# Kernel tuning notes

Measured on AMD Instinct MI355X. Metric: run time of the kernel, lower is better.

The kernel has to match this reference:

```python
import math
import jax, jax.numpy as jnp
import numpy as np

D_MODEL = 1024
D_K = 64
D_V = 64
N_HEADS = 16
D_HIDDEN = 4096
EPS = 1e-5


def setup_inputs() -> dict:
    key = jax.random.key(0)
    ks = jax.random.split(key, 10)
    s = 0.02
    x = jax.random.normal(ks[0], (2, 2048, D_MODEL), dtype=jnp.float32)
    wq = jax.random.normal(ks[1], (D_MODEL, D_K * N_HEADS), jnp.float32) * s
    bq = jnp.zeros((D_K * N_HEADS,), jnp.float32)
    wk = jax.random.normal(ks[2], (D_MODEL, D_K * N_HEADS), jnp.float32) * s
    bk = jnp.zeros((D_K * N_HEADS,), jnp.float32)
    wv = jax.random.normal(ks[3], (D_MODEL, D_V * N_HEADS), jnp.float32) * s
    bv = jnp.zeros((D_V * N_HEADS,), jnp.float32)
    wo = jax.random.normal(ks[4], (D_V * N_HEADS, D_MODEL), jnp.float32) * s
    ln1_g = jnp.ones((D_MODEL,), jnp.float32)
    ln1_b = jnp.zeros((D_MODEL,), jnp.float32)
    w1 = jax.random.normal(ks[5], (D_MODEL, D_HIDDEN), jnp.float32) * s
    b1 = jnp.zeros((D_HIDDEN,), jnp.float32)
    w2 = jax.random.normal(ks[6], (D_HIDDEN, D_MODEL), jnp.float32) * s
    ln2_g = jnp.ones((D_MODEL,), jnp.float32)
    ln2_b = jnp.zeros((D_MODEL,), jnp.float32)
    return dict(x=x, wq=wq, bq=bq, wk=wk, bk=bk, wv=wv, bv=bv, wo=wo,
                ln1_g=ln1_g, ln1_b=ln1_b, w1=w1, b1=b1, w2=w2,
                ln2_g=ln2_g, ln2_b=ln2_b)


def _layernorm(x, g, b):
    mu = jnp.mean(x, axis=-1, keepdims=True)
    var = jnp.mean((x - mu) ** 2, axis=-1, keepdims=True)
    return (x - mu) * jax.lax.rsqrt(var + EPS) * g + b


def reference(x, wq, bq, wk, bk, wv, bv, wo, ln1_g, ln1_b, w1, b1, w2, ln2_g, ln2_b):
    B, S, _ = x.shape
    split = lambda t, d: t.reshape(B, S, N_HEADS, d).transpose(0, 2, 1, 3)  # [B,H,S,d]
    Q = split(x @ wq + bq, D_K)
    K = split(x @ wk + bk, D_K)
    V = split(x @ wv + bv, D_V)
    scores = jnp.einsum('bhqd,bhkd->bhqk', Q / math.sqrt(D_K), K)
    causal = jnp.tril(jnp.ones((S, S), dtype=bool))
    scores = jnp.where(causal, scores, -jnp.inf)
    attn = jax.nn.softmax(scores, axis=-1)
    ctx = jnp.einsum('bhqk,bhkd->bhqd', attn, V)  # [B,H,S,d_v]
    merged = ctx.transpose(0, 2, 1, 3).reshape(B, S, N_HEADS * D_V)
    x = x + _layernorm(merged @ wo, ln1_g, ln1_b)
    h = jax.nn.gelu(x @ w1 + b1, approximate=False)
    x = x + _layernorm(h @ w2, ln2_g, ln2_b)
    return x
```

## Files before the change

kernel.cpp:

```cpp
#include <hip/hip_runtime.h>
#include <math.h>

typedef __bf16 bf16;
typedef __bf16 bf16x4 __attribute__((ext_vector_type(4)));
typedef __bf16 bf16x8 __attribute__((ext_vector_type(8)));
typedef float f32x4 __attribute__((ext_vector_type(4)));

#define MFMA16(a, b, c) __builtin_amdgcn_mfma_f32_16x16x32_bf16(a, b, c, 0, 0, 0)
#define QSCALE 0.180336879f
#define SSTR 3072

typedef __attribute__((address_space(3))) unsigned int lds_uint;
typedef const __attribute__((address_space(1))) unsigned int glb_uint;
__device__ __forceinline__ void gload_lds16(const void* g, void* l) {
    __builtin_amdgcn_global_load_lds((glb_uint*)g, (lds_uint*)l, 16, 0, 0);
}

__global__ __launch_bounds__(256) void prep_kernel(
    const float* __restrict__ x,
    const float* __restrict__ wq, const float* __restrict__ wk,
    const float* __restrict__ wv, const float* __restrict__ wo,
    const float* __restrict__ w1, const float* __restrict__ w2,
    const float* __restrict__ bq, const float* __restrict__ bk,
    const float* __restrict__ bv,
    bf16* __restrict__ xbf, bf16* __restrict__ wqkvt, bf16* __restrict__ wot,
    bf16* __restrict__ w1t, bf16* __restrict__ w2t, float* __restrict__ bqkv) {
    const int bid = blockIdx.x, tid = threadIdx.x;
    if (bid < 4096) {
        size_t i = ((size_t)bid * 256 + tid) * 4;
        float4 v = *(const float4*)(x + i);
        bf16x4 o = {(bf16)v.x, (bf16)v.y, (bf16)v.z, (bf16)v.w};
        *(bf16x4*)(xbf + i) = o;
        return;
    }
    if (bid < 16384) {
        __shared__ float tile[32][33];
        const float* W; bf16* Wt; int K, N, n0, k0;
        if (bid < 8192) {
            int l = bid - 4096, z = l >> 10, t = l & 1023;
            W = z == 0 ? wq : z == 1 ? wk : z == 2 ? wv : wo;
            Wt = z == 3 ? wot : wqkvt + (size_t)z * 1024 * 1024;
            K = 1024; N = 1024; n0 = (t & 31) * 32; k0 = (t >> 5) * 32;
        } else if (bid < 12288) {
            int l = bid - 8192;
            W = w1; Wt = w1t; K = 1024; N = 4096;
            n0 = (l & 127) * 32; k0 = (l >> 7) * 32;
        } else {
            int l = bid - 12288;
            W = w2; Wt = w2t; K = 4096; N = 1024;
            n0 = (l & 31) * 32; k0 = (l >> 5) * 32;
        }
        const int tx = tid & 31, ty = tid >> 5;
        for (int i = 0; i < 32; i += 8)
            tile[ty + i][tx] = W[(size_t)(k0 + ty + i) * N + n0 + tx];
        __syncthreads();
        for (int i = 0; i < 32; i += 8)
            Wt[(size_t)(n0 + ty + i) * K + k0 + tx] = (bf16)tile[tx][ty + i];
        return;
    }
    int i = (bid - 16384) * 256 + tid;
    bqkv[i] = i < 1024 ? bq[i] : i < 2048 ? bk[i - 1024] : bv[i - 2048];
}

__global__ void transpose_v_kernel(const bf16* __restrict__ QKV, bf16* __restrict__ Vtg) {
    __shared__ bf16 t[64 * 64];
    const int tid = threadIdx.x;
    const int st = blockIdx.x;
    const int bh = blockIdx.y;
    const int b = bh >> 4, h = bh & 15;
    const bf16* src = QKV + (size_t)b * 2048 * SSTR + 2048 + h * 64 + (size_t)st * 64 * SSTR;
    const int s = tid >> 3, oct = tid & 7;
    bf16x8 v0 = *(const bf16x8*)&src[(size_t)s * SSTR + oct * 8];
    bf16x8 v1 = *(const bf16x8*)&src[(size_t)(s + 32) * SSTR + oct * 8];
    *(bf16x8*)&t[s * 64 + ((oct ^ (s & 7)) * 8)] = v0;
    *(bf16x8*)&t[(s + 32) * 64 + ((oct ^ (s & 7)) * 8)] = v1;
    __syncthreads();
    const int dv = tid >> 3, so = tid & 7;
    bf16 b0[8], b1[8];
#pragma unroll
    for (int j = 0; j < 8; j++) {
        int ss = so * 8 + j;
        b0[j] = t[ss * 64 + (((dv >> 3) ^ (ss & 7)) * 8) + (dv & 7)];
        b1[j] = t[ss * 64 + ((((dv + 32) >> 3) ^ (ss & 7)) * 8) + (dv & 7)];
    }
    bf16* dst = Vtg + (size_t)bh * 64 * 2048 + (size_t)st * 64;
    *(bf16x8*)&dst[(size_t)dv * 2048 + so * 8] = *(bf16x8*)b0;
    *(bf16x8*)&dst[(size_t)(dv + 32) * 2048 + so * 8] = *(bf16x8*)b1;
}

template <bool HAS_BIAS, bool DO_GELU, bool OUT_BF16, bool QKV_SCALE, int NSPLIT>
__global__ __launch_bounds__(256, 4) void gemm_nt(
    const bf16* __restrict__ A, const bf16* __restrict__ Bt,
    const float* __restrict__ bias,
    float* __restrict__ Cf, bf16* __restrict__ Cb,
    int M, int N, int K) {
    __shared__ bf16 As[2][128 * 32];
    __shared__ bf16 Bs[2][128 * 32];
    const int tid = threadIdx.x;
    const int wave = tid >> 6, lane = tid & 63;
    const int ln = lane & 15, quad = lane >> 4;
    const int GN = N >> 7;
    const int nblk = gridDim.x;
    const int bid = blockIdx.x;
    const int lid = (bid & 7) * (nblk >> 3) + (bid >> 3);
    const int ngroup = GN * 8;
    const int g = lid / ngroup, rem = lid - g * ngroup;
    const int m0 = (g * 8 + (rem & 7)) * 128;
    const int n0 = (rem >> 3) * 128;
    const int wm = (wave >> 1) * 64, wn = (wave & 1) * 64;
    int kz0 = 0, kz1 = K;
    if (NSPLIT > 1) {
        const int kchunk = K / NSPLIT;
        kz0 = blockIdx.z * kchunk;
        kz1 = kz0 + kchunk;
        if (OUT_BF16) Cb += (size_t)blockIdx.z * M * N;
        else          Cf += (size_t)blockIdx.z * M * N;
    }
    const int srow0 = wave * 32 + (lane >> 2);
    const int srow1 = srow0 + 16;
    const int soct = ((lane & 3) ^ (srow0 & 3)) * 8;
    const bf16* ga0 = A + (size_t)(m0 + srow0) * K + soct;
    const bf16* ga1 = A + (size_t)(m0 + srow1) * K + soct;
    const bf16* gb0 = Bt + (size_t)(n0 + srow0) * K + soct;
    const bf16* gb1 = Bt + (size_t)(n0 + srow1) * K + soct;

    f32x4 acc[4][4] = {};
    const int roct = (quad ^ (ln & 3)) * 8;

#define GSTAGE(k0_, bi_)                                        \
    {                                                           \
        bf16* la = As[bi_] + wave * 1024;                       \
        bf16* lb = Bs[bi_] + wave * 1024;                       \
        gload_lds16(ga0 + (k0_), la);                           \
        gload_lds16(ga1 + (k0_), la + 512);                     \
        gload_lds16(gb0 + (k0_), lb);                           \
        gload_lds16(gb1 + (k0_), lb + 512);                     \
    }

    GSTAGE(kz0, 0)
    int it = 0;
    for (int k0 = kz0; k0 < kz1; k0 += 32, ++it) {
        const int cur = it & 1;
        __syncthreads();
        if (k0 + 32 < kz1) GSTAGE(k0 + 32, cur ^ 1)
        bf16x8 af[4], bg[4];
#pragma unroll
        for (int i = 0; i < 4; i++) {
            af[i] = *(const bf16x8*)&As[cur][(wm + i * 16 + ln) * 32 + roct];
            bg[i] = *(const bf16x8*)&Bs[cur][(wn + i * 16 + ln) * 32 + roct];
        }
#pragma unroll
        for (int i = 0; i < 4; i++)
#pragma unroll
            for (int j = 0; j < 4; j++)
                acc[i][j] = MFMA16(af[i], bg[j], acc[i][j]);
    }
#undef GSTAGE

#pragma unroll
    for (int i = 0; i < 4; i++)
#pragma unroll
        for (int j = 0; j < 4; j++) {
            int col = n0 + wn + j * 16 + ln;
            float bv = HAS_BIAS ? bias[col] : 0.0f;
#pragma unroll
            for (int r = 0; r < 4; r++) {
                int row = m0 + wm + i * 16 + quad * 4 + r;
                float v = acc[i][j][r] + bv;
                if (QKV_SCALE && col < 1024) v *= QSCALE;
                if (DO_GELU) {
                    float u = v * (v * v * 0.044715f + 1.0f) * 0.7978845608f;
                    float t = __builtin_amdgcn_exp2f(u * 2.885390082f);
                    v = v * t * __builtin_amdgcn_rcpf(t + 1.0f);
                }
                if (OUT_BF16)
                    Cb[(size_t)row * N + col] = (bf16)v;
                else
                    Cf[(size_t)row * N + col] = v;
            }
        }
}

__global__ __launch_bounds__(256, 4) void attn_kernel(
    const bf16* __restrict__ QKV, const bf16* __restrict__ Vtg,
    bf16* __restrict__ ctx) {
    __shared__ bf16 Ks[2][64 * 64];
    __shared__ bf16 Vs[2][64 * 64];
    const int tid = threadIdx.x, wave = tid >> 6, lane = tid & 63;
    const int ln = lane & 15, quad = lane >> 4;
    const int idx = blockIdx.x;
    const int qt = 31 - (idx >> 5);
    const int bh = idx & 31;
    const int b = bh >> 4, h = bh & 15;
    const size_t qkvbase = (size_t)b * 2048 * SSTR;
    const bf16* Qp = QKV + qkvbase + h * 64;
    const bf16* Kp = QKV + qkvbase + 1024 + h * 64;
    const bf16* Vtp = Vtg + (size_t)bh * 64 * 2048;
    const int qw = qt * 64 + wave * 16;
    const int qg = qw + ln;

    bf16x8 bq0 = *(const bf16x8*)&Qp[(size_t)qg * SSTR + quad * 8];
    bf16x8 bq1 = *(const bf16x8*)&Qp[(size_t)qg * SSTR + 32 + quad * 8];

    f32x4 o[4] = {};
    float m_run = -__builtin_inff(), l_run = 0.0f;

    const int kr = wave * 16 + (lane >> 3);
    const int koct = ((lane & 7) ^ (kr & 7)) * 8;
    const bf16* gk0 = Kp + (size_t)kr * SSTR + koct;
    const bf16* gk1 = Kp + (size_t)(kr + 8) * SSTR + koct;
    const bf16* gv0 = Vtp + (size_t)kr * 2048 + koct;
    const bf16* gv1 = Vtp + (size_t)(kr + 8) * 2048 + koct;

    const int nkt = qt + 1;
#define STAGE(kt_, bi_)                                                     \
    {                                                                       \
        const int kk = (kt_) * 64;                                          \
        bf16* lk = Ks[bi_] + wave * 1024;                                   \
        bf16* lv = Vs[bi_] + wave * 1024;                                   \
        gload_lds16(gk0 + (size_t)kk * SSTR, lk);                           \
        gload_lds16(gk1 + (size_t)kk * SSTR, lk + 512);                     \
        gload_lds16(gv0 + kk, lv);                                          \
        gload_lds16(gv1 + kk, lv + 512);                                    \
    }

    STAGE(0, 0)
    for (int kt = 0; kt < nkt; kt++) {
        const int cur = kt & 1;
        const int k0 = kt * 64;
        __syncthreads();
        if (kt + 1 < nkt) STAGE(kt + 1, cur ^ 1)

        const bf16* Kc = Ks[cur];
        const bf16* Vc = Vs[cur];
        f32x4 sc[4] = {};
#pragma unroll
        for (int mt = 0; mt < 4; mt++) {
            const int sk = mt * 16 + ln, s7 = sk & 7;
            bf16x8 ka0 = *(const bf16x8*)&Kc[sk * 64 + ((quad ^ s7) * 8)];
            bf16x8 ka1 = *(const bf16x8*)&Kc[sk * 64 + (((quad + 4) ^ s7) * 8)];
            sc[mt] = MFMA16(ka0, bq0, sc[mt]);
            sc[mt] = MFMA16(ka1, bq1, sc[mt]);
        }
        if (kt == qt) {
#pragma unroll
            for (int mt = 0; mt < 4; mt++)
#pragma unroll
                for (int r = 0; r < 4; r++) {
                    const int kg = k0 + mt * 16 + quad * 4 + r;
                    if (kg > qg) sc[mt][r] = -__builtin_inff();
                }
        }
        float mx = m_run;
#pragma unroll
        for (int mt = 0; mt < 4; mt++)
#pragma unroll
            for (int r = 0; r < 4; r++) mx = fmaxf(mx, sc[mt][r]);
        mx = fmaxf(mx, __shfl_xor(mx, 16));
        mx = fmaxf(mx, __shfl_xor(mx, 32));
        const float alpha = __builtin_amdgcn_exp2f(m_run - mx);
        m_run = mx;
        float sum = 0.0f;
#pragma unroll
        for (int mt = 0; mt < 4; mt++)
#pragma unroll
            for (int r = 0; r < 4; r++) {
                float pv = __builtin_amdgcn_exp2f(sc[mt][r] - mx);
                sc[mt][r] = pv;
                sum += pv;
            }
        l_run = l_run * alpha + sum;
#pragma unroll
        for (int nt = 0; nt < 4; nt++) o[nt] *= alpha;

        bf16x8 pb0, pb1;
#pragma unroll
        for (int r = 0; r < 4; r++) {
            pb0[r]     = (bf16)sc[0][r];
            pb0[r + 4] = (bf16)sc[1][r];
            pb1[r]     = (bf16)sc[2][r];
            pb1[r + 4] = (bf16)sc[3][r];
        }
        const int q2 = quad >> 1, q4 = (quad & 1) * 4;
#pragma unroll
        for (int nt = 0; nt < 4; nt++) {
            const int row = nt * 16 + ln, r7 = row & 7;
            bf16x4 v0 = *(const bf16x4*)&Vc[row * 64 + ((q2 ^ r7) * 8) + q4];
            bf16x4 v1 = *(const bf16x4*)&Vc[row * 64 + (((q2 + 2) ^ r7) * 8) + q4];
            bf16x4 v2 = *(const bf16x4*)&Vc[row * 64 + (((q2 + 4) ^ r7) * 8) + q4];
            bf16x4 v3 = *(const bf16x4*)&Vc[row * 64 + (((q2 + 6) ^ r7) * 8) + q4];
            bf16x8 va0, va1;
#pragma unroll
            for (int r = 0; r < 4; r++) {
                va0[r] = v0[r]; va0[r + 4] = v1[r];
                va1[r] = v2[r]; va1[r + 4] = v3[r];
            }
            o[nt] = MFMA16(va0, pb0, o[nt]);
            o[nt] = MFMA16(va1, pb1, o[nt]);
        }
    }
#undef STAGE

    __syncthreads();
    l_run += __shfl_xor(l_run, 16);
    l_run += __shfl_xor(l_run, 32);
    const float inv = 1.0f / l_run;

    bf16* Ob = Ks[0] + wave * 1024;
#pragma unroll
    for (int nt = 0; nt < 4; nt++)
#pragma unroll
        for (int r = 0; r < 4; r++) {
            const int dvh = 2 * nt + (quad >> 1);
            const int dlo = (quad & 1) * 4 + r;
            Ob[ln * 64 + ((dvh ^ (ln & 7)) * 8) + dlo] = (bf16)(o[nt][r] * inv);
        }
    bf16* ctxp = ctx + (size_t)b * 2048 * 1024 + h * 64;
#pragma unroll
    for (int p2 = 0; p2 < 2; p2++) {
        const int qL = (lane >> 3) + 8 * p2;
        const int oct = lane & 7;
        bf16x8 v = *(const bf16x8*)&Ob[qL * 64 + ((oct ^ (qL & 7)) * 8)];
        *(bf16x8*)&ctxp[(size_t)(qw + qL) * 1024 + oct * 8] = v;
    }
}

template <int NPART>
__global__ __launch_bounds__(256) void ln_res_kernel(
    const float* res, const bf16* __restrict__ yb,
    const float* __restrict__ g, const float* __restrict__ beta,
    float* outf, bf16* __restrict__ outb) {
    const int row = blockIdx.x;
    const int tid = threadIdx.x;
    const size_t off = (size_t)row * 1024 + tid * 4;
    const size_t pstride = (size_t)4096 * 1024;
    float4 v = {0.0f, 0.0f, 0.0f, 0.0f};
#pragma unroll
    for (int pi = 0; pi < NPART; pi++) {
        bf16x4 a = *(const bf16x4*)(yb + pi * pstride + off);
        v.x += (float)a[0]; v.y += (float)a[1];
        v.z += (float)a[2]; v.w += (float)a[3];
    }
    float s = v.x + v.y + v.z + v.w;
    float s2 = v.x * v.x + v.y * v.y + v.z * v.z + v.w * v.w;
#pragma unroll
    for (int o = 1; o < 64; o <<= 1) {
        s += __shfl_xor(s, o);
        s2 += __shfl_xor(s2, o);
    }
    __shared__ float ws[8];
    const int wave = tid >> 6, lane = tid & 63;
    if (lane == 0) { ws[wave] = s; ws[4 + wave] = s2; }
    __syncthreads();
    s = ws[0] + ws[1] + ws[2] + ws[3];
    s2 = ws[4] + ws[5] + ws[6] + ws[7];
    float mu = s * (1.0f / 1024.0f);
    float var = s2 * (1.0f / 1024.0f) - mu * mu;
    float rs = rsqrtf(var + 1e-5f);
    float4 gv = *(const float4*)(g + tid * 4);
    float4 bv = *(const float4*)(beta + tid * 4);
    float4 rv = *(const float4*)(res + off);
    float4 ov;
    ov.x = rv.x + (v.x - mu) * rs * gv.x + bv.x;
    ov.y = rv.y + (v.y - mu) * rs * gv.y + bv.y;
    ov.z = rv.z + (v.z - mu) * rs * gv.z + bv.z;
    ov.w = rv.w + (v.w - mu) * rs * gv.w + bv.w;
    *(float4*)(outf + off) = ov;
    if (outb) {
        bf16x4 ob = {(bf16)ov.x, (bf16)ov.y, (bf16)ov.z, (bf16)ov.w};
        *(bf16x4*)(outb + off) = ob;
    }
}


extern "C" void kernel_launch(void* const* d_in, const int* in_sizes, int n_in,
                              void* d_out, int out_size, void* d_ws, size_t ws_size,
                              hipStream_t stream) {
    const float* x  = (const float*)d_in[0];
    const float* wq = (const float*)d_in[1];
    const float* bq = (const float*)d_in[2];
    const float* wk = (const float*)d_in[3];
    const float* bk = (const float*)d_in[4];
    const float* wv = (const float*)d_in[5];
    const float* bv = (const float*)d_in[6];
    const float* wo = (const float*)d_in[7];
    const float* g1 = (const float*)d_in[8];
    const float* be1 = (const float*)d_in[9];
    const float* w1 = (const float*)d_in[10];
    const float* b1 = (const float*)d_in[11];
    const float* w2 = (const float*)d_in[12];
    const float* g2 = (const float*)d_in[13];
    const float* be2 = (const float*)d_in[14];
    float* out = (float*)d_out;

    const int T = 4096;
    char* p = (char*)d_ws;
    auto take = [&](size_t n) { char* r = p; p += n; return r; };
    bf16* xbf   = (bf16*)take((size_t)T * 1024 * 2);
    bf16* wqkvt = (bf16*)take((size_t)3072 * 1024 * 2);
    float* bqkv = (float*)take(3072 * 4 + 4096);
    bf16* wot   = (bf16*)take(1024 * 1024 * 2);
    bf16* w1t   = (bf16*)take((size_t)4096 * 1024 * 2);
    bf16* w2t   = (bf16*)take((size_t)1024 * 4096 * 2);
    bf16* QKV   = (bf16*)take((size_t)T * 3072 * 2);
    bf16* ctx   = (bf16*)take((size_t)T * 1024 * 2);
    bf16* ypart = (bf16*)take((size_t)2 * T * 1024 * 2);
    bf16* Vtg   = (bf16*)take((size_t)32 * 64 * 2048 * 2);
    take((size_t)T * 1024 * 2);
    bf16* h   = QKV;
    bf16* x1b = xbf;
    float* x1 = out;

    prep_kernel<<<16396, 256, 0, stream>>>(x, wq, wk, wv, wo, w1, w2, bq, bk, bv,
                                           xbf, wqkvt, wot, w1t, w2t, bqkv);

    gemm_nt<true, false, true, true, 1><<<768, 256, 0, stream>>>(
        xbf, wqkvt, bqkv, nullptr, QKV, T, 3072, 1024);

    transpose_v_kernel<<<dim3(32, 32), 256, 0, stream>>>(QKV, Vtg);
    attn_kernel<<<1024, 256, 0, stream>>>(QKV, Vtg, ctx);

    gemm_nt<false, false, true, false, 2><<<dim3(256, 1, 2), 256, 0, stream>>>(
        ctx, wot, nullptr, nullptr, ypart, T, 1024, 1024);

    ln_res_kernel<2><<<T, 256, 0, stream>>>(x, ypart, g1, be1, x1, x1b);

    gemm_nt<true, true, true, false, 1><<<1024, 256, 0, stream>>>(
        x1b, w1t, b1, nullptr, h, T, 4096, 1024);

    gemm_nt<false, false, true, false, 4><<<dim3(256, 1, 4), 256, 0, stream>>>(
        h, w2t, nullptr, nullptr, ypart, T, 1024, 4096);

    ln_res_kernel<4><<<T, 256, 0, stream>>>(x1, ypart, g2, be2, out, nullptr);
}
```

Measured before the change: 335.0 us.

## Add 256x256 eight-wave GEMM with fine-grained prefetch schedule for QKV and FFN

Adds a new 256x256-tile GEMM kernel with 512 threads, double-buffered LDS (128KB), inline-asm ds_read_b128, interleaved global-to-LDS loads split into quarter-tile stages, explicit barriers, vmcnt waits and s_setprio around MFMA bursts. It is used for the QKV projection and both FFN GEMMs. The aim is higher arithmetic intensity per LDS byte and better overlap of memory with MFMA. Separately, the attention kernel raises wave priority around its MFMA loops. Risks include fewer blocks than CUs for some grids (192, 256 blocks), the occupancy limits that come with 128KB LDS, and a fragile hand-written wait schedule.

```diff
diff --git a/kernel.cpp b/kernel.cpp
--- a/kernel.cpp
+++ b/kernel.cpp
@@ -14,6 +14,9 @@
 typedef const __attribute__((address_space(1))) unsigned int glb_uint;
 __device__ __forceinline__ void gload_lds16(const void* g, void* l) {
     __builtin_amdgcn_global_load_lds((glb_uint*)g, (lds_uint*)l, 16, 0, 0);
+}
+__device__ __forceinline__ unsigned lds_addr(const void* p) {
+    return (unsigned)(unsigned long long)(lds_uint*)p;
 }
 
 __global__ __launch_bounds__(256) void prep_kernel(
@@ -181,6 +184,171 @@
         }
 }
 
+#define BARR() __builtin_amdgcn_s_barrier()
+#define WAITDS() { asm volatile("s_waitcnt lgkmcnt(0)" ::: "memory"); \
+                   __builtin_amdgcn_sched_barrier(0); }
+#define WAITVM4() asm volatile("s_waitcnt vmcnt(4)" ::: "memory")
+#define WAITVM0() asm volatile("s_waitcnt vmcnt(0)" ::: "memory")
+#define PRIO1() __builtin_amdgcn_s_setprio(1)
+#define PRIO0() __builtin_amdgcn_s_setprio(0)
+#define DSR(d_, a_, o_) asm volatile("ds_read_b128 %0, %1 offset:%2" \
+                                     : "=v"(d_) : "v"(a_), "i"(o_))
+
+__device__ __forceinline__ void mfma_q(f32x4 (&acc)[8][4], const bf16x8 (&aF)[4][2],
+                                       const bf16x8 (&bR)[2][2], int IO, int NO) {
+#pragma unroll
+    for (int i = 0; i < 4; i++)
+#pragma unroll
+        for (int n = 0; n < 2; n++) {
+            acc[IO + i][NO + n] = MFMA16(aF[i][0], bR[n][0], acc[IO + i][NO + n]);
+            acc[IO + i][NO + n] = MFMA16(aF[i][1], bR[n][1], acc[IO + i][NO + n]);
+        }
+}
+
+template <bool HAS_BIAS, bool DO_GELU, bool QKV_SCALE, int NSPLIT>
+__global__ __launch_bounds__(512, 2) void gemm256(
+    const bf16* __restrict__ A, const bf16* __restrict__ Bt,
+    const float* __restrict__ bias, bf16* __restrict__ Cb,
+    int M, int N, int K) {
+    __shared__ bf16 sh[65536];
+    const int tid = threadIdx.x;
+    const int wave = tid >> 6, lane = tid & 63;
+    const int ln = lane & 15, quad = lane >> 4;
+    const int wm = (wave >> 2) * 128, wn = (wave & 3) * 64;
+    const int GN = N >> 8;
+    const int nblk = gridDim.x;
+    const int bid = blockIdx.x;
+    const int lid = (bid & 7) * (nblk >> 3) + (bid >> 3);
+    const int ngroup = GN * 8;
+    const int gg = lid / ngroup, rem = lid - gg * ngroup;
+    const int m0 = (gg * 8 + (rem & 7)) * 256;
+    const int n0 = (rem >> 3) * 256;
+    int kz0 = 0, KS = K;
+    if (NSPLIT > 1) {
+        KS = K / NSPLIT;
+        kz0 = blockIdx.z * KS;
+        Cb += (size_t)blockIdx.z * M * N;
+    }
+    const int NT = KS >> 6;
+
+    const int lr = lane >> 3, lc = lane & 7;
+    const int co = (lc ^ lr) * 8;
+    const int hg0 = wave * 16 + lr, hg1 = hg0 + 8;
+    const int rA0g0 = hg0 + (hg0 >= 64 ? 64 : 0);
+    const int rA0g1 = hg1 + (hg1 >= 64 ? 64 : 0);
+    const int rB0g0 = (hg0 >> 5) * 64 + (hg0 & 31);
+    const int rB0g1 = (hg1 >> 5) * 64 + (hg1 & 31);
+    const bf16* gA0 = A + (size_t)(m0 + rA0g0) * K + kz0 + co;
+    const bf16* gA1 = A + (size_t)(m0 + rA0g1) * K + kz0 + co;
+    const bf16* gB0 = Bt + (size_t)(n0 + rB0g0) * K + kz0 + co;
+    const bf16* gB1 = Bt + (size_t)(n0 + rB0g1) * K + kz0 + co;
+    const size_t aoff64 = (size_t)64 * K;
+    const size_t boff32 = (size_t)32 * K;
+    const int hA0 = wave * 16, hA1 = wave * 16 + 8;
+    const int R0A0 = hA0 + (hA0 >= 64 ? 64 : 0);
+    const int R0A1 = hA1 + (hA1 >= 64 ? 64 : 0);
+    const int R0B0 = (hA0 >> 5) * 64 + (hA0 & 31);
+    const int R0B1 = (hA1 >> 5) * 64 + (hA1 & 31);
+
+#define ST_A0(B_, T_) do { \
+    gload_lds16(gA0 + (size_t)(T_) * 64, sh + (B_) * 16384 + R0A0 * 64); \
+    gload_lds16(gA1 + (size_t)(T_) * 64, sh + (B_) * 16384 + R0A1 * 64); } while (0)
+#define ST_A1(B_, T_) do { \
+    gload_lds16(gA0 + aoff64 + (size_t)(T_) * 64, sh + (B_) * 16384 + 4096 + R0A0 * 64); \
+    gload_lds16(gA1 + aoff64 + (size_t)(T_) * 64, sh + (B_) * 16384 + 4096 + R0A1 * 64); } while (0)
+#define ST_B0(B_, T_) do { \
+    gload_lds16(gB0 + (size_t)(T_) * 64, sh + 32768 + (B_) * 16384 + R0B0 * 64); \
+    gload_lds16(gB1 + (size_t)(T_) * 64, sh + 32768 + (B_) * 16384 + R0B1 * 64); } while (0)
+#define ST_B1(B_, T_) do { \
+    gload_lds16(gB0 + boff32 + (size_t)(T_) * 64, sh + 32768 + (B_) * 16384 + 2048 + R0B0 * 64); \
+    gload_lds16(gB1 + boff32 + (size_t)(T_) * 64, sh + 32768 + (B_) * 16384 + 2048 + R0B1 * 64); } while (0)
+
+    const unsigned lb = lds_addr(sh);
+    unsigned aAdr[2][2], bAdr[2][2];
+#pragma unroll
+    for (int bu = 0; bu < 2; bu++)
+#pragma unroll
+        for (int ks = 0; ks < 2; ks++) {
+            unsigned sw = (unsigned)(((ks * 4 + quad) ^ (ln & 7)) * 16);
+            aAdr[bu][ks] = lb + bu * 32768u + (unsigned)(wm + ln) * 128u + sw;
+            bAdr[bu][ks] = lb + 65536u + bu * 32768u + (unsigned)(wn + ln) * 128u + sw;
+        }
+
+    f32x4 acc[8][4] = {};
+    bf16x8 aF[4][2], bQ0[2][2], bQ1[2][2];
+
+    ST_A0(0, 0); ST_B0(0, 0); ST_A1(0, 0); ST_B1(0, 0);
+    ST_A0(1, 1); ST_B0(1, 1);
+    WAITVM4();
+    BARR();
+
+#define TILE(B_, U_) { \
+     \
+    DSR(aF[0][0], aAdr[B_][0], 0);     DSR(aF[0][1], aAdr[B_][1], 0); \
+    DSR(aF[1][0], aAdr[B_][0], 2048);  DSR(aF[1][1], aAdr[B_][1], 2048); \
+    DSR(aF[2][0], aAdr[B_][0], 4096);  DSR(aF[2][1], aAdr[B_][1], 4096); \
+    DSR(aF[3][0], aAdr[B_][0], 6144);  DSR(aF[3][1], aAdr[B_][1], 6144); \
+    DSR(bQ0[0][0], bAdr[B_][0], 0);    DSR(bQ0[0][1], bAdr[B_][1], 0); \
+    DSR(bQ0[1][0], bAdr[B_][0], 2048); DSR(bQ0[1][1], bAdr[B_][1], 2048); \
+    if ((U_) + 1 < NT) ST_A1((B_) ^ 1, (U_) + 1); \
+    BARR(); WAITDS(); PRIO1(); \
+    mfma_q(acc, aF, bQ0, 0, 0); \
+    PRIO0(); BARR(); \
+     \
+    DSR(bQ1[0][0], bAdr[B_][0], 4096); DSR(bQ1[0][1], bAdr[B_][1], 4096); \
+    DSR(bQ1[1][0], bAdr[B_][0], 6144); DSR(bQ1[1][1], bAdr[B_][1], 6144); \
+    if ((U_) + 1 < NT) ST_B1((B_) ^ 1, (U_) + 1); \
+    BARR(); WAITDS(); PRIO1(); \
+    mfma_q(acc, aF, bQ1, 0, 2); \
+    PRIO0(); BARR(); \
+     \
+    DSR(aF[0][0], aAdr[B_][0], 8192);  DSR(aF[0][1], aAdr[B_][1], 8192); \
+    DSR(aF[1][0], aAdr[B_][0], 10240); DSR(aF[1][1], aAdr[B_][1], 10240); \
+    DSR(aF[2][0], aAdr[B_][0], 12288); DSR(aF[2][1], aAdr[B_][1], 12288); \
+    DSR(aF[3][0], aAdr[B_][0], 14336); DSR(aF[3][1], aAdr[B_][1], 14336); \
+    if ((U_) + 2 < NT) ST_A0(B_, (U_) + 2); \
+    BARR(); WAITDS(); PRIO1(); \
+    mfma_q(acc, aF, bQ0, 4, 0); \
+    PRIO0(); BARR(); \
+     \
+    if ((U_) + 2 < NT) ST_B0(B_, (U_) + 2); \
+    if ((U_) == NT - 2) { WAITVM0(); } else { WAITVM4(); } \
+    BARR(); PRIO1(); \
+    mfma_q(acc, aF, bQ1, 4, 2); \
+    PRIO0(); BARR(); \
+}
+
+    for (int u = 0; u < NT; u += 2) {
+        TILE(0, u)
+        TILE(1, u + 1)
+    }
+#undef TILE
+#undef ST_A0
+#undef ST_A1
+#undef ST_B0
+#undef ST_B1
+
+#pragma unroll
+    for (int i = 0; i < 8; i++)
+#pragma unroll
+        for (int j = 0; j < 4; j++) {
+            int col = n0 + wn + j * 16 + ln;
+            float bvv = HAS_BIAS ? bias[col] : 0.0f;
+#pragma unroll
+            for (int rr = 0; rr < 4; rr++) {
+                int row = m0 + wm + i * 16 + quad * 4 + rr;
+                float v = acc[i][j][rr] + bvv;
+                if (QKV_SCALE && col < 1024) v *= QSCALE;
+                if (DO_GELU) {
+                    float u = v * (v * v * 0.044715f + 1.0f) * 0.7978845608f;
+                    float t = __builtin_amdgcn_exp2f(u * 2.885390082f);
+                    v = v * t * __builtin_amdgcn_rcpf(t + 1.0f);
+                }
+                Cb[(size_t)row * N + col] = (bf16)v;
+            }
+        }
+}
+
 __global__ __launch_bounds__(256, 4) void attn_kernel(
     const bf16* __restrict__ QKV, const bf16* __restrict__ Vtg,
     bf16* __restrict__ ctx) {
@@ -234,6 +402,7 @@
         const bf16* Kc = Ks[cur];
         const bf16* Vc = Vs[cur];
         f32x4 sc[4] = {};
+        __builtin_amdgcn_s_setprio(1);
 #pragma unroll
         for (int mt = 0; mt < 4; mt++) {
             const int sk = mt * 16 + ln, s7 = sk & 7;
@@ -242,6 +411,7 @@
             sc[mt] = MFMA16(ka0, bq0, sc[mt]);
             sc[mt] = MFMA16(ka1, bq1, sc[mt]);
         }
+        __builtin_amdgcn_s_setprio(0);
         if (kt == qt) {
 #pragma unroll
             for (int mt = 0; mt < 4; mt++)
@@ -282,6 +452,7 @@
             pb1[r + 4] = (bf16)sc[3][r];
         }
         const int q2 = quad >> 1, q4 = (quad & 1) * 4;
+        __builtin_amdgcn_s_setprio(1);
 #pragma unroll
         for (int nt = 0; nt < 4; nt++) {
             const int row = nt * 16 + ln, r7 = row & 7;
@@ -298,6 +469,7 @@
             o[nt] = MFMA16(va0, pb0, o[nt]);
             o[nt] = MFMA16(va1, pb1, o[nt]);
         }
+        __builtin_amdgcn_s_setprio(0);
     }
 #undef STAGE
 
@@ -414,8 +586,8 @@
     prep_kernel<<<16396, 256, 0, stream>>>(x, wq, wk, wv, wo, w1, w2, bq, bk, bv,
                                            xbf, wqkvt, wot, w1t, w2t, bqkv);
 
-    gemm_nt<true, false, true, true, 1><<<768, 256, 0, stream>>>(
-        xbf, wqkvt, bqkv, nullptr, QKV, T, 3072, 1024);
+    gemm256<true, false, true, 1><<<192, 512, 0, stream>>>(
+        xbf, wqkvt, bqkv, QKV, T, 3072, 1024);
 
     transpose_v_kernel<<<dim3(32, 32), 256, 0, stream>>>(QKV, Vtg);
     attn_kernel<<<1024, 256, 0, stream>>>(QKV, Vtg, ctx);
@@ -425,11 +597,11 @@
 
     ln_res_kernel<2><<<T, 256, 0, stream>>>(x, ypart, g1, be1, x1, x1b);
 
-    gemm_nt<true, true, true, false, 1><<<1024, 256, 0, stream>>>(
-        x1b, w1t, b1, nullptr, h, T, 4096, 1024);
-
-    gemm_nt<false, false, true, false, 4><<<dim3(256, 1, 4), 256, 0, stream>>>(
-        h, w2t, nullptr, nullptr, ypart, T, 1024, 4096);
+    gemm256<true, true, false, 1><<<256, 512, 0, stream>>>(
+        x1b, w1t, b1, h, T, 4096, 1024);
+
+    gemm256<false, false, false, 4><<<dim3(64, 1, 4), 512, 0, stream>>>(
+        h, w2t, nullptr, ypart, T, 1024, 4096);
 
     ln_res_kernel<4><<<T, 256, 0, stream>>>(x1, ypart, g2, be2, out, nullptr);
 }
```

New measurement: 323.7 us. -3.4%, faster.
